# Performance work log

Measured on AMD Instinct MI355X. Metric: run time of the kernel, lower is better.

## Reference

```python
import jax, jax.numpy as jnp
import numpy as np

N = 100000
E = 1600000
IN_DIM = 128
HEADS = 4
OUT_DIM = 32


def setup_inputs() -> dict:
    key = jax.random.key(0)
    k1, k2, k3, k4, k5 = jax.random.split(key, 5)
    x = jax.random.normal(k1, (N, IN_DIM), dtype=jnp.float32)
    edge_index = jax.random.randint(k2, (2, E), 0, N, dtype=jnp.int64)
    # torch Linear weight: (out_features, in_features) = (HEADS*OUT_DIM, IN_DIM)
    W = jax.random.normal(k3, (HEADS * OUT_DIM, IN_DIM), dtype=jnp.float32) * 0.05
    a_src = jax.random.normal(k4, (HEADS, OUT_DIM), dtype=jnp.float32)
    a_dst = jax.random.normal(k5, (HEADS, OUT_DIM), dtype=jnp.float32)
    return {"x": x, "edge_index": edge_index, "W": W, "a_src": a_src, "a_dst": a_dst}


def reference(x, edge_index, W, a_src, a_dst):
    n = x.shape[0]
    H, D = a_src.shape
    # h: (N, H, D)
    h = (x @ W.T).reshape(n, H, D)
    src, dst = edge_index[0], edge_index[1]
    # per-edge attention logits: (E, H)
    e_src = jnp.einsum('ehd,hd->eh', h[src], a_src)
    e_dst = jnp.einsum('ehd,hd->eh', h[dst], a_dst)
    e = jax.nn.leaky_relu(e_src + e_dst, negative_slope=0.2)
    # segment max per destination node (init zeros, include_self=True as in torch)
    e_max = jnp.zeros((n, H), dtype=x.dtype).at[dst].max(e)
    e_exp = jnp.exp(e - e_max[dst])
    e_sum = jnp.zeros((n, H), dtype=x.dtype).at[dst].add(e_exp)
    alpha = e_exp / (e_sum[dst] + 1e-8)  # (E, H)
    # weighted messages and scatter-add aggregation
    msg = h[src] * alpha[..., None]  # (E, H, D)
    out = jnp.zeros((n, H, D), dtype=x.dtype).at[dst].add(msg)
    return out.reshape(n, H * D)  # concat=True
```

## Files before the change

### kernel.cpp

```cpp
#include <hip/hip_runtime.h>

#define IN_DIM 128
#define HD 128
#define HEADS 4
#define MD 64
#define CAP 128
#define NCOHORT 8
#define CHUNK 2048
#define NBMAX 512

typedef float nf4  __attribute__((ext_vector_type(4)));
typedef unsigned short nu4 __attribute__((ext_vector_type(4)));

__device__ __forceinline__ float lrelu(float v){ return v > 0.f ? v : 0.2f*v; }
__device__ __forceinline__ float4 add4(float4 a, float4 b){
  return make_float4(a.x+b.x, a.y+b.y, a.z+b.z, a.w+b.w);
}
__device__ __forceinline__ float4 expl4(float4 v){
  return make_float4(__expf(lrelu(v.x)), __expf(lrelu(v.y)), __expf(lrelu(v.z)), __expf(lrelu(v.w)));
}
__device__ __forceinline__ unsigned short f2b(float f){
  unsigned u = __float_as_uint(f);
  return (unsigned short)((u + 0x7FFFu + ((u >> 16) & 1u)) >> 16);
}
__device__ __forceinline__ float b2f(unsigned short b){
  return __uint_as_float(((unsigned)b) << 16);
}
__device__ __forceinline__ float blo(unsigned u){ return __uint_as_float(u << 16); }
__device__ __forceinline__ float bhi(unsigned u){ return __uint_as_float(u & 0xFFFF0000u); }

__global__ __launch_bounds__(256) void k_init(const float* __restrict__ W, float* __restrict__ WT){
  int idx = blockIdx.x*256 + threadIdx.x;
  int j = idx >> 7, k = idx & 127;
  WT[k*128 + j] = W[idx];
}

__global__ __launch_bounds__(256) void k_gemm_only(
    const float* __restrict__ x, const float* __restrict__ WT,
    const float* __restrict__ a_src, const float* __restrict__ a_dst,
    unsigned short* __restrict__ h, float* __restrict__ s, float* __restrict__ t,
    int n_nodes){
  __shared__ float xs[32][132];
  const int tid = threadIdx.x;
  const int base = blockIdx.x*32;
  if (base >= n_nodes) return;
  const int jg  = tid & 31;
  const int ng  = tid >> 5;
  const int j4  = jg*4;
  const float4 as4 = *(const float4*)(a_src + j4);
  const float4 ad4 = *(const float4*)(a_dst + j4);

  for (int i = tid; i < 32*32; i += 256){
    int row = i >> 5, c4 = (i & 31)*4;
    nf4 v = {0.f,0.f,0.f,0.f};
    if (base + row < n_nodes)
      v = __builtin_nontemporal_load((const nf4*)(x + (size_t)(base+row)*IN_DIM + c4));
    *(nf4*)&xs[row][c4] = v;
  }
  __syncthreads();

  float acc[4][4];
  #pragma unroll
  for (int i=0;i<4;++i){ acc[i][0]=acc[i][1]=acc[i][2]=acc[i][3]=0.f; }
  const int nb = ng*4;
  const float* wp = WT + j4;

  float4 wc0 = *(const float4*)(wp);
  float4 wc1 = *(const float4*)(wp + 128);
  float4 wc2 = *(const float4*)(wp + 256);
  float4 wc3 = *(const float4*)(wp + 384);
  for (int k=0;k<128;k+=4){
    const float* wq = wp + (size_t)(((k+4) & 127))*128;
    float4 wn0 = *(const float4*)(wq);
    float4 wn1 = *(const float4*)(wq + 128);
    float4 wn2 = *(const float4*)(wq + 256);
    float4 wn3 = *(const float4*)(wq + 384);
    #pragma unroll
    for (int u=0;u<4;++u){
      float4 xv = *(const float4*)&xs[nb+u][k];
      acc[u][0] = fmaf(wc0.x, xv.x, acc[u][0]);
      acc[u][1] = fmaf(wc0.y, xv.x, acc[u][1]);
      acc[u][2] = fmaf(wc0.z, xv.x, acc[u][2]);
      acc[u][3] = fmaf(wc0.w, xv.x, acc[u][3]);
      acc[u][0] = fmaf(wc1.x, xv.y, acc[u][0]);
      acc[u][1] = fmaf(wc1.y, xv.y, acc[u][1]);
      acc[u][2] = fmaf(wc1.z, xv.y, acc[u][2]);
      acc[u][3] = fmaf(wc1.w, xv.y, acc[u][3]);
      acc[u][0] = fmaf(wc2.x, xv.z, acc[u][0]);
      acc[u][1] = fmaf(wc2.y, xv.z, acc[u][1]);
      acc[u][2] = fmaf(wc2.z, xv.z, acc[u][2]);
      acc[u][3] = fmaf(wc2.w, xv.z, acc[u][3]);
      acc[u][0] = fmaf(wc3.x, xv.w, acc[u][0]);
      acc[u][1] = fmaf(wc3.y, xv.w, acc[u][1]);
      acc[u][2] = fmaf(wc3.z, xv.w, acc[u][2]);
      acc[u][3] = fmaf(wc3.w, xv.w, acc[u][3]);
    }
    wc0 = wn0; wc1 = wn1; wc2 = wn2; wc3 = wn3;
  }

  #pragma unroll
  for (int i=0;i<4;++i){
    int node = base + nb + i;
    if (node < n_nodes){
      nu4 hv = { f2b(acc[i][0]), f2b(acc[i][1]), f2b(acc[i][2]), f2b(acc[i][3]) };
      __builtin_nontemporal_store(hv, (nu4*)(h + (size_t)node*HD + j4));
    }
  }
  #pragma unroll
  for (int i=0;i<4;++i){
    float ps = acc[i][0]*as4.x + acc[i][1]*as4.y + acc[i][2]*as4.z + acc[i][3]*as4.w;
    float pt = acc[i][0]*ad4.x + acc[i][1]*ad4.y + acc[i][2]*ad4.z + acc[i][3]*ad4.w;
    ps += __shfl_xor(ps,1,64); ps += __shfl_xor(ps,2,64); ps += __shfl_xor(ps,4,64);
    pt += __shfl_xor(pt,1,64); pt += __shfl_xor(pt,2,64); pt += __shfl_xor(pt,4,64);
    if ((jg & 7) == 0){
      int node = base + nb + i;
      if (node < n_nodes){
        int hh = jg >> 3;
        s[node*HEADS + hh] = ps;
        t[node*HEADS + hh] = pt;
      }
    }
  }
}

__global__ __launch_bounds__(256) void k_bcount(const int* __restrict__ edst, int E_,
                                                int* __restrict__ cmat, int NB){
  __shared__ int hist[NBMAX];
  const int tid = threadIdx.x;
  for (int b = tid; b < NB; b += 256) hist[b] = 0;
  __syncthreads();
  const int base = blockIdx.x*CHUNK;
  const int lim  = (base + CHUNK < E_) ? base + CHUNK : E_;
  for (int i = base + tid; i < lim; i += 256)
    atomicAdd(&hist[((unsigned)edst[i]) >> 8], 1);
  __syncthreads();
  for (int b = tid; b < NB; b += 256)
    cmat[(size_t)blockIdx.x*NB + b] = hist[b];
}

__global__ __launch_bounds__(256) void k_bscan(int* __restrict__ cmat, int NCH, int NB,
                                               int* __restrict__ btot){
  const int lane = threadIdx.x & 63;
  const int b = blockIdx.x*4 + (threadIdx.x >> 6);
  if (b >= NB) return;
  int run = 0;
  for (int c0 = 0; c0 < NCH; c0 += 64){
    int c = c0 + lane;
    int v = (c < NCH) ? cmat[(size_t)c*NB + b] : 0;
    int incl = v;
    #pragma unroll
    for (int o=1;o<64;o<<=1){ int u = __shfl_up(incl, o, 64); if (lane >= o) incl += u; }
    if (c < NCH) cmat[(size_t)c*NB + b] = run + incl - v;
    run += __shfl(incl, 63, 64);
  }
  if (lane == 0) btot[b] = run;
}

__global__ __launch_bounds__(64) void k_bbase(const int* __restrict__ btot, int NB,
                                              int* __restrict__ bbase){
  const int lane = threadIdx.x;
  int run = 0;
  for (int c0 = 0; c0 < NB; c0 += 64){
    int c = c0 + lane;
    int v = (c < NB) ? btot[c] : 0;
    int incl = v;
    #pragma unroll
    for (int o=1;o<64;o<<=1){ int u = __shfl_up(incl, o, 64); if (lane >= o) incl += u; }
    if (c < NB) bbase[c] = run + incl - v;
    run += __shfl(incl, 63, 64);
  }
  if (lane == 0) bbase[NB] = run;
}

__global__ __launch_bounds__(256) void k_bscatter(const int* __restrict__ esrc,
    const int* __restrict__ edst, int E_, const int* __restrict__ cmat,
    const int* __restrict__ bbase, int* __restrict__ bucketbuf, int NB){
  __shared__ int cur[NBMAX];
  const int tid = threadIdx.x;
  for (int b = tid; b < NB; b += 256)
    cur[b] = bbase[b] + cmat[(size_t)blockIdx.x*NB + b];
  __syncthreads();
  const int base = blockIdx.x*CHUNK;
  const int lim  = (base + CHUNK < E_) ? base + CHUNK : E_;
  for (int i = base + tid; i < lim; i += 256){
    unsigned d = (unsigned)edst[i];
    int b = d >> 8;
    int pos = atomicAdd(&cur[b], 1);
    bucketbuf[pos] = esrc[i] | ((int)(d & 255u) << 24);
  }
}

__global__ __launch_bounds__(256) void k_bslots(const int* __restrict__ bucketbuf,
    const int* __restrict__ bbase, int* __restrict__ slots, int* __restrict__ count,
    int n_nodes){
  __shared__ int ncnt[256];
  const int tid = threadIdx.x;
  const int b = blockIdx.x;
  const int lo = bbase[b], hi = bbase[b+1];
  ncnt[tid] = 0;
  __syncthreads();
  for (int i = lo + tid; i < hi; i += 256)
    atomicAdd(&ncnt[((unsigned)bucketbuf[i]) >> 24], 1);
  __syncthreads();
  int node = b*256 + tid;
  if (node < n_nodes) count[node] = ncnt[tid];
  __syncthreads();
  ncnt[tid] = 0;
  __syncthreads();
  for (int i = lo + tid; i < hi; i += 256){
    int p = bucketbuf[i];
    int ld = ((unsigned)p) >> 24;
    int pos = atomicAdd(&ncnt[ld], 1);
    if (pos < MD) slots[(size_t)(b*256 + ld)*MD + pos] = p & 0xFFFFFF;
  }
}

__global__ __launch_bounds__(256) void k_aggregate2(const int* __restrict__ slots,
    const int* __restrict__ count, const unsigned short* __restrict__ h,
    const float* __restrict__ s, const float* __restrict__ t,
    float* __restrict__ out, int n_nodes){
  __shared__ int   s_src[4][MD];
  __shared__ float s_exp[4][MD][4];
  const int lane = threadIdx.x & 63;
  const int slot = threadIdx.x >> 6;
  const int n = blockIdx.x*4 + slot;
  if (n >= n_nodes) return;
  int cnt = count[n]; if (cnt > MD) cnt = MD;
  const float4 t4 = *(const float4*)(t + n*HEADS);

  float4 z4 = make_float4(0.f,0.f,0.f,0.f);
  if (lane < cnt){
    int src = slots[(size_t)n*MD + lane];
    s_src[slot][lane] = src;
    float4 s4 = *(const float4*)(s + src*HEADS);
    float4 e4 = expl4(add4(s4, t4));
    z4 = e4;
    *(float4*)&s_exp[slot][lane][0] = e4;
  }
  #pragma unroll
  for (int o=1;o<64;o<<=1){
    z4.x += __shfl_xor(z4.x,o,64);
    z4.y += __shfl_xor(z4.y,o,64);
    z4.z += __shfl_xor(z4.z,o,64);
    z4.w += __shfl_xor(z4.w,o,64);
  }

  const int qtr = lane >> 4;
  const int q   = lane & 15;
  const int hd  = q >> 2;
  float zh = hd==0 ? z4.x : hd==1 ? z4.y : hd==2 ? z4.z : z4.w;
  const float r = 1.f/(zh + 1e-8f);
  float4 accA = make_float4(0.f,0.f,0.f,0.f);
  float4 accB = make_float4(0.f,0.f,0.f,0.f);
  const unsigned short* hq = h + 8*q;

#define FMA8(U, W) \
  accA.x = fmaf(W, blo(U.x), accA.x); accA.y = fmaf(W, bhi(U.x), accA.y); \
  accA.z = fmaf(W, blo(U.y), accA.z); accA.w = fmaf(W, bhi(U.y), accA.w); \
  accB.x = fmaf(W, blo(U.z), accB.x); accB.y = fmaf(W, bhi(U.z), accB.y); \
  accB.z = fmaf(W, blo(U.w), accB.z); accB.w = fmaf(W, bhi(U.w), accB.w);

  int i = 0;
  for (; i + 8 <= cnt; i += 8){
    int eA = i + qtr, eB = i + 4 + qtr;
    int aA = s_src[slot][eA], aB = s_src[slot][eB];
    uint4 uA = *(const uint4*)(hq + (size_t)aA*HD);
    uint4 uB = *(const uint4*)(hq + (size_t)aB*HD);
    float wA = s_exp[slot][eA][hd], wB = s_exp[slot][eB][hd];
    FMA8(uA, wA); FMA8(uB, wB);
  }
  if (i + 4 <= cnt){
    int eA = i + qtr;
    int aA = s_src[slot][eA];
    uint4 uA = *(const uint4*)(hq + (size_t)aA*HD);
    float wA = s_exp[slot][eA][hd];
    FMA8(uA, wA);
    i += 4;
  }
  if (i < cnt && qtr < cnt - i){
    int eA = i + qtr;
    int aA = s_src[slot][eA];
    uint4 uA = *(const uint4*)(hq + (size_t)aA*HD);
    float wA = s_exp[slot][eA][hd];
    FMA8(uA, wA);
  }
#undef FMA8

  #pragma unroll
  for (int o=16;o<64;o<<=1){
    accA.x += __shfl_xor(accA.x,o,64); accA.y += __shfl_xor(accA.y,o,64);
    accA.z += __shfl_xor(accA.z,o,64); accA.w += __shfl_xor(accA.w,o,64);
    accB.x += __shfl_xor(accB.x,o,64); accB.y += __shfl_xor(accB.y,o,64);
    accB.z += __shfl_xor(accB.z,o,64); accB.w += __shfl_xor(accB.w,o,64);
  }
  if (qtr == 0){
    *(float4*)(out + (size_t)n*HD + 8*q)     = make_float4(accA.x*r, accA.y*r, accA.z*r, accA.w*r);
    *(float4*)(out + (size_t)n*HD + 8*q + 4) = make_float4(accB.x*r, accB.y*r, accB.z*r, accB.w*r);
  }
}

__global__ __launch_bounds__(256) void k_gemm(const float* __restrict__ x, const float* __restrict__ WT,
    const float* __restrict__ a_src, const float* __restrict__ a_dst,
    unsigned short* __restrict__ h, float* __restrict__ s, float* __restrict__ t,
    int n_nodes, int n_tiles){
  __shared__ float xs[64][132];
  const int tid = threadIdx.x;
  const int jg  = tid & 31;
  const int ng  = tid >> 5;
  const int j4  = jg*4;
  const float4 as4 = *(const float4*)(a_src + j4);
  const float4 ad4 = *(const float4*)(a_dst + j4);

  for (int tile = blockIdx.x; tile < n_tiles; tile += gridDim.x){
    const int base = tile*64;
    __syncthreads();
    for (int i = tid; i < 64*32; i += 256){
      int row = i >> 5, c4 = (i & 31)*4;
      float4 v = make_float4(0.f,0.f,0.f,0.f);
      if (base + row < n_nodes) v = *(const float4*)(x + (size_t)(base+row)*IN_DIM + c4);
      *(float4*)&xs[row][c4] = v;
    }
    __syncthreads();

    float acc[8][4];
    #pragma unroll
    for (int i=0;i<8;++i){ acc[i][0]=acc[i][1]=acc[i][2]=acc[i][3]=0.f; }
    const int nb = ng*8;
    for (int k=0;k<128;k+=4){
      float4 w0 = *(const float4*)(WT + (k  )*128 + j4);
      float4 w1 = *(const float4*)(WT + (k+1)*128 + j4);
      float4 w2 = *(const float4*)(WT + (k+2)*128 + j4);
      float4 w3 = *(const float4*)(WT + (k+3)*128 + j4);
      #pragma unroll
      for (int i=0;i<8;++i){
        float4 xv = *(const float4*)&xs[nb+i][k];
        acc[i][0] = fmaf(w0.x, xv.x, acc[i][0]); acc[i][1] = fmaf(w0.y, xv.x, acc[i][1]);
        acc[i][2] = fmaf(w0.z, xv.x, acc[i][2]); acc[i][3] = fmaf(w0.w, xv.x, acc[i][3]);
        acc[i][0] = fmaf(w1.x, xv.y, acc[i][0]); acc[i][1] = fmaf(w1.y, xv.y, acc[i][1]);
        acc[i][2] = fmaf(w1.z, xv.y, acc[i][2]); acc[i][3] = fmaf(w1.w, xv.y, acc[i][3]);
        acc[i][0] = fmaf(w2.x, xv.z, acc[i][0]); acc[i][1] = fmaf(w2.y, xv.z, acc[i][1]);
        acc[i][2] = fmaf(w2.z, xv.z, acc[i][2]); acc[i][3] = fmaf(w2.w, xv.z, acc[i][3]);
        acc[i][0] = fmaf(w3.x, xv.w, acc[i][0]); acc[i][1] = fmaf(w3.y, xv.w, acc[i][1]);
        acc[i][2] = fmaf(w3.z, xv.w, acc[i][2]); acc[i][3] = fmaf(w3.w, xv.w, acc[i][3]);
      }
    }
    #pragma unroll
    for (int i=0;i<8;++i){
      int node = base + nb + i;
      if (node < n_nodes)
        *(ushort4*)(h + (size_t)node*HD + j4) =
          make_ushort4(f2b(acc[i][0]), f2b(acc[i][1]), f2b(acc[i][2]), f2b(acc[i][3]));
    }
    #pragma unroll
    for (int i=0;i<8;++i){
      float ps = acc[i][0]*as4.x + acc[i][1]*as4.y + acc[i][2]*as4.z + acc[i][3]*as4.w;
      float pt = acc[i][0]*ad4.x + acc[i][1]*ad4.y + acc[i][2]*ad4.z + acc[i][3]*ad4.w;
      ps += __shfl_xor(ps,1,64); ps += __shfl_xor(ps,2,64); ps += __shfl_xor(ps,4,64);
      pt += __shfl_xor(pt,1,64); pt += __shfl_xor(pt,2,64); pt += __shfl_xor(pt,4,64);
      if ((jg & 7) == 0){
        int node = base + nb + i;
        if (node < n_nodes){
          int hh = jg >> 3;
          s[node*HEADS + hh] = ps;
          t[node*HEADS + hh] = pt;
        }
      }
    }
  }
}

__global__ __launch_bounds__(256) void k_hist(const int* __restrict__ dst, int E_,
                                              int* __restrict__ count, int R){
  const int c  = blockIdx.x & (NCOHORT-1);
  const int g  = (blockIdx.x >> 3)*256 + threadIdx.x;
  const int gs = (gridDim.x >> 3)*256;
  const unsigned lo = (unsigned)(c*R);
  for (int e = g; e < E_; e += gs){
    unsigned d = (unsigned)dst[e];
    if (d - lo < (unsigned)R) atomicAdd(&count[d], 1);
  }
}

__global__ void k_offsets(const int* __restrict__ count, int n_nodes,
                          int* __restrict__ offs, int* __restrict__ wcur, int* __restrict__ cursor){
  int n = blockIdx.x*blockDim.x + threadIdx.x;
  int lane = threadIdx.x & 63;
  int c = (n < n_nodes) ? count[n] : 0;
  int incl = c;
  #pragma unroll
  for (int o=1;o<64;o<<=1){
    int v = __shfl_up(incl, o, 64);
    if (lane >= o) incl += v;
  }
  int wave_total = __shfl(incl, 63, 64);
  int base = 0;
  if (lane == 63) base = atomicAdd(cursor, wave_total);
  base = __shfl(base, 63, 64);
  if (n < n_nodes){
    int off = base + incl - c;
    offs[n] = off; wcur[n] = off;
  }
}

__global__ __launch_bounds__(256) void k_scatter(const int* __restrict__ src, const int* __restrict__ dst,
                                                 int E_, int* __restrict__ wcur,
                                                 int* __restrict__ csr_src, int R){
  const int c  = blockIdx.x & (NCOHORT-1);
  const int g  = (blockIdx.x >> 3)*256 + threadIdx.x;
  const int gs = (gridDim.x >> 3)*256;
  const unsigned lo = (unsigned)(c*R);
  for (int e = g; e < E_; e += gs){
    unsigned d = (unsigned)dst[e];
    if (d - lo < (unsigned)R){
      int pos = atomicAdd(&wcur[d], 1);
      csr_src[pos] = src[e];
    }
  }
}

__global__ __launch_bounds__(256) void k_aggregate(const int* __restrict__ csr_src,
    const int* __restrict__ offs, const int* __restrict__ count,
    const unsigned short* __restrict__ h, const float* __restrict__ s, const float* __restrict__ t,
    float* __restrict__ out, int n_nodes){
  __shared__ int   s_src[4][CAP];
  __shared__ float s_exp[4][CAP][4];
  const int lane = threadIdx.x & 63;
  const int slot = threadIdx.x >> 6;
  const int n = blockIdx.x*4 + slot;
  if (n >= n_nodes) return;
  const int start = offs[n];
  const int cnt   = count[n];
  const float4 t4 = *(const float4*)(t + n*HEADS);
  const bool fast = (cnt <= CAP);

  float4 z4 = make_float4(0.f,0.f,0.f,0.f);
  if (fast){
    #pragma unroll
    for (int j=0;j<2;++j){
      int i = lane + j*64;
      if (i < cnt){
        int src = csr_src[start+i];
        s_src[slot][i] = src;
        float4 s4 = *(const float4*)(s + src*HEADS);
        float4 e4 = expl4(add4(s4, t4));
        z4 = add4(z4, e4);
        *(float4*)&s_exp[slot][i][0] = e4;
      }
    }
  } else {
    for (int i = lane; i < cnt; i += 64){
      int src = csr_src[start+i];
      float4 s4 = *(const float4*)(s + src*HEADS);
      z4 = add4(z4, expl4(add4(s4, t4)));
    }
  }
  #pragma unroll
  for (int o=1;o<64;o<<=1){
    z4.x += __shfl_xor(z4.x,o,64);
    z4.y += __shfl_xor(z4.y,o,64);
    z4.z += __shfl_xor(z4.z,o,64);
    z4.w += __shfl_xor(z4.w,o,64);
  }

  if (fast){
    const int half = lane >> 5;
    const int fl   = lane & 31;
    const int hd   = fl >> 3;
    float zh = hd==0 ? z4.x : hd==1 ? z4.y : hd==2 ? z4.z : z4.w;
    const float r = 1.f/(zh + 1e-8f);
    float4 acc = make_float4(0.f,0.f,0.f,0.f);
    int i = 0;
    for (; i + 4 <= cnt; i += 4){
      int a0 = s_src[slot][i+half], a1 = s_src[slot][i+2+half];
      ushort4 u0 = *(const ushort4*)(h + (size_t)a0*HD + 4*fl);
      ushort4 u1 = *(const ushort4*)(h + (size_t)a1*HD + 4*fl);
      float e0 = s_exp[slot][i+half][hd], e1 = s_exp[slot][i+2+half][hd];
      acc.x = fmaf(e0, b2f(u0.x), acc.x); acc.y = fmaf(e0, b2f(u0.y), acc.y);
      acc.z = fmaf(e0, b2f(u0.z), acc.z); acc.w = fmaf(e0, b2f(u0.w), acc.w);
      acc.x = fmaf(e1, b2f(u1.x), acc.x); acc.y = fmaf(e1, b2f(u1.y), acc.y);
      acc.z = fmaf(e1, b2f(u1.z), acc.z); acc.w = fmaf(e1, b2f(u1.w), acc.w);
    }
    if (i + 2 <= cnt){
      int a0 = s_src[slot][i+half];
      ushort4 u0 = *(const ushort4*)(h + (size_t)a0*HD + 4*fl);
      float e0 = s_exp[slot][i+half][hd];
      acc.x = fmaf(e0, b2f(u0.x), acc.x); acc.y = fmaf(e0, b2f(u0.y), acc.y);
      acc.z = fmaf(e0, b2f(u0.z), acc.z); acc.w = fmaf(e0, b2f(u0.w), acc.w);
      i += 2;
    }
    if (i < cnt && half == 0){
      int a0 = s_src[slot][i];
      ushort4 u0 = *(const ushort4*)(h + (size_t)a0*HD + 4*fl);
      float e0 = s_exp[slot][i][hd];
      acc.x = fmaf(e0, b2f(u0.x), acc.x); acc.y = fmaf(e0, b2f(u0.y), acc.y);
      acc.z = fmaf(e0, b2f(u0.z), acc.z); acc.w = fmaf(e0, b2f(u0.w), acc.w);
    }
    acc.x += __shfl_xor(acc.x, 32, 64);
    acc.y += __shfl_xor(acc.y, 32, 64);
    acc.z += __shfl_xor(acc.z, 32, 64);
    acc.w += __shfl_xor(acc.w, 32, 64);
    if (half == 0){
      *(float4*)(out + (size_t)n*HD + 4*fl) = make_float4(acc.x*r, acc.y*r, acc.z*r, acc.w*r);
    }
  } else {
    const int hd = lane >> 4;
    float zh = hd==0 ? z4.x : hd==1 ? z4.y : hd==2 ? z4.z : z4.w;
    const float r = 1.f/(zh + 1e-8f);
    float th = hd==0 ? t4.x : hd==1 ? t4.y : hd==2 ? t4.z : t4.w;
    float2 acc = make_float2(0.f,0.f);
    for (int i = 0; i < cnt; ++i){
      int src = csr_src[start+i];
      float4 s4 = *(const float4*)(s + src*HEADS);
      float sh = hd==0 ? s4.x : hd==1 ? s4.y : hd==2 ? s4.z : s4.w;
      float e = __expf(lrelu(sh+th));
      ushort2 u = *(const ushort2*)(h + (size_t)src*HD + 2*lane);
      acc.x = fmaf(e, b2f(u.x), acc.x); acc.y = fmaf(e, b2f(u.y), acc.y);
    }
    *(float2*)(out + (size_t)n*HD + 2*lane) = make_float2(acc.x*r, acc.y*r);
  }
}

extern "C" void kernel_launch(void* const* d_in, const int* in_sizes, int n_in,
                              void* d_out, int out_size, void* d_ws, size_t ws_size,
                              hipStream_t stream) {
  const float* x     = (const float*)d_in[0];
  const int*   ei    = (const int*)d_in[1];
  const float* W     = (const float*)d_in[2];
  const float* a_src = (const float*)d_in[3];
  const float* a_dst = (const float*)d_in[4];
  float* out = (float*)d_out;

  const int n_nodes = in_sizes[0] / IN_DIM;
  const int E_      = in_sizes[1] / 2;
  const int R       = (n_nodes + NCOHORT - 1) / NCOHORT;
  const int NB      = (n_nodes + 255) >> 8;
  const int NCH     = (E_ + CHUNK - 1) / CHUNK;

  char* ws = (char*)d_ws;
  size_t off = 0;
  auto alloc = [&](size_t bytes){ size_t cur = off; off += (bytes + 255) & ~255ULL; return cur; };

  float*          WT = (float*)(ws + alloc(128*128*4));
  unsigned short* h  = (unsigned short*)(ws + alloc((size_t)n_nodes*HD*2));
  float*          s  = (float*)(ws + alloc((size_t)n_nodes*HEADS*4));
  float*          t  = (float*)(ws + alloc((size_t)n_nodes*HEADS*4));

  size_t ms_need = off
    + (((size_t)n_nodes*4       + 255) & ~255ULL)
    + (((size_t)n_nodes*MD*4    + 255) & ~255ULL)
    + (((size_t)NCH*NB*4        + 255) & ~255ULL)
    + (((size_t)NB*4            + 255) & ~255ULL)
    + (((size_t)(NB+1)*4        + 255) & ~255ULL)
    + (((size_t)E_*4            + 255) & ~255ULL);

  if (ws_size >= ms_need && NB <= NBMAX && n_nodes < (1 << 24)){
    int* count     = (int*)(ws + alloc((size_t)n_nodes*4));
    int* slots     = (int*)(ws + alloc((size_t)n_nodes*MD*4));
    int* cmat      = (int*)(ws + alloc((size_t)NCH*NB*4));
    int* btot      = (int*)(ws + alloc((size_t)NB*4));
    int* bbase     = (int*)(ws + alloc((size_t)(NB+1)*4));
    int* bucketbuf = (int*)(ws + alloc((size_t)E_*4));

    k_init<<<64, 256, 0, stream>>>(W, WT);
    k_gemm_only<<<(n_nodes+31)/32, 256, 0, stream>>>(x, WT, a_src, a_dst, h, s, t, n_nodes);
    k_bcount<<<NCH, 256, 0, stream>>>(ei + E_, E_, cmat, NB);
    k_bscan<<<(NB+3)/4, 256, 0, stream>>>(cmat, NCH, NB, btot);
    k_bbase<<<1, 64, 0, stream>>>(btot, NB, bbase);
    k_bscatter<<<NCH, 256, 0, stream>>>(ei, ei + E_, E_, cmat, bbase, bucketbuf, NB);
    k_bslots<<<NB, 256, 0, stream>>>(bucketbuf, bbase, slots, count, n_nodes);
    k_aggregate2<<<(n_nodes+3)/4, 256, 0, stream>>>(slots, count, h, s, t, out, n_nodes);
  } else {
    int* count   = (int*)(ws + alloc((size_t)n_nodes*4));
    int* offs    = (int*)(ws + alloc((size_t)n_nodes*4));
    int* wcur    = (int*)(ws + alloc((size_t)n_nodes*4));
    int* cursor  = (int*)(ws + alloc(4));
    int* csr_src = (int*)(ws + alloc((size_t)E_*4));
    const int n_tiles = (n_nodes + 63) / 64;

    hipMemsetAsync(count, 0, (size_t)n_nodes*4, stream);
    hipMemsetAsync(cursor, 0, 4, stream);
    k_init<<<64, 256, 0, stream>>>(W, WT);
    k_gemm<<<n_tiles, 256, 0, stream>>>(x, WT, a_src, a_dst, h, s, t, n_nodes, n_tiles);
    k_hist<<<2048, 256, 0, stream>>>(ei + E_, E_, count, R);
    k_offsets<<<(n_nodes+255)/256, 256, 0, stream>>>(count, n_nodes, offs, wcur, cursor);
    k_scatter<<<2048, 256, 0, stream>>>(ei, ei + E_, E_, wcur, csr_src, R);
    k_aggregate<<<(n_nodes+3)/4, 256, 0, stream>>>(csr_src, offs, count, h, s, t, out, n_nodes);
  }
}
```

Before: 200.6 us.

## Interleave GEMM tiles into bucket-sort kernels and fold bbase scan into consumers

The standalone GEMM kernel is split into tiles and distributed across the four bucket-sort phase kernels as extra blocks. The GEMM work then runs alongside the latency-bound histogram, scan, scatter and slot kernels, filling idle compute units. The separate single-block bbase scan kernel is removed, and each scatter and slots block recomputes the bucket base prefix in shared memory. This saves launches but adds redundant per-block scans and extra shared memory that may lower occupancy.

```diff
diff --git a/kernel.cpp b/kernel.cpp
--- a/kernel.cpp
+++ b/kernel.cpp
@@ -35,14 +35,12 @@
   WT[k*128 + j] = W[idx];
 }
 
-__global__ __launch_bounds__(256) void k_gemm_only(
+__device__ __forceinline__ void gemm_tile(int tile,
     const float* __restrict__ x, const float* __restrict__ WT,
     const float* __restrict__ a_src, const float* __restrict__ a_dst,
     unsigned short* __restrict__ h, float* __restrict__ s, float* __restrict__ t,
-    int n_nodes){
-  __shared__ float xs[32][132];
-  const int tid = threadIdx.x;
-  const int base = blockIdx.x*32;
+    int n_nodes, float (*xs)[132], int tid){
+  const int base = tile*32;
   if (base >= n_nodes) return;
   const int jg  = tid & 31;
   const int ng  = tid >> 5;
@@ -123,95 +121,137 @@
   }
 }
 
-__global__ __launch_bounds__(256) void k_bcount(const int* __restrict__ edst, int E_,
-                                                int* __restrict__ cmat, int NB){
+__device__ __forceinline__ void scan_bbase(const int* __restrict__ btot, int NB,
+                                           int* bb, int tid){
+  if (tid < 64){
+    int run = 0;
+    for (int c0 = 0; c0 < NB; c0 += 64){
+      int c = c0 + tid;
+      int v = (c < NB) ? btot[c] : 0;
+      int incl = v;
+      #pragma unroll
+      for (int o=1;o<64;o<<=1){ int u = __shfl_up(incl, o, 64); if (tid >= o) incl += u; }
+      if (c < NB) bb[c] = run + incl - v;
+      run += __shfl(incl, 63, 64);
+    }
+    if (tid == 0) bb[NB] = run;
+  }
+  __syncthreads();
+}
+
+__global__ __launch_bounds__(256) void k_p1(const int* __restrict__ edst, int E_,
+    int* __restrict__ cmat, int NB, int NCH,
+    const float* __restrict__ x, const float* __restrict__ WT,
+    const float* __restrict__ a_src, const float* __restrict__ a_dst,
+    unsigned short* __restrict__ h, float* __restrict__ s, float* __restrict__ t,
+    int n_nodes, int g_base){
+  __shared__ float xs[32][132];
   __shared__ int hist[NBMAX];
   const int tid = threadIdx.x;
-  for (int b = tid; b < NB; b += 256) hist[b] = 0;
-  __syncthreads();
-  const int base = blockIdx.x*CHUNK;
-  const int lim  = (base + CHUNK < E_) ? base + CHUNK : E_;
-  for (int i = base + tid; i < lim; i += 256)
-    atomicAdd(&hist[((unsigned)edst[i]) >> 8], 1);
-  __syncthreads();
-  for (int b = tid; b < NB; b += 256)
-    cmat[(size_t)blockIdx.x*NB + b] = hist[b];
-}
-
-__global__ __launch_bounds__(256) void k_bscan(int* __restrict__ cmat, int NCH, int NB,
-                                               int* __restrict__ btot){
-  const int lane = threadIdx.x & 63;
-  const int b = blockIdx.x*4 + (threadIdx.x >> 6);
-  if (b >= NB) return;
-  int run = 0;
-  for (int c0 = 0; c0 < NCH; c0 += 64){
-    int c = c0 + lane;
-    int v = (c < NCH) ? cmat[(size_t)c*NB + b] : 0;
-    int incl = v;
-    #pragma unroll
-    for (int o=1;o<64;o<<=1){ int u = __shfl_up(incl, o, 64); if (lane >= o) incl += u; }
-    if (c < NCH) cmat[(size_t)c*NB + b] = run + incl - v;
-    run += __shfl(incl, 63, 64);
-  }
-  if (lane == 0) btot[b] = run;
-}
-
-__global__ __launch_bounds__(64) void k_bbase(const int* __restrict__ btot, int NB,
-                                              int* __restrict__ bbase){
-  const int lane = threadIdx.x;
-  int run = 0;
-  for (int c0 = 0; c0 < NB; c0 += 64){
-    int c = c0 + lane;
-    int v = (c < NB) ? btot[c] : 0;
-    int incl = v;
-    #pragma unroll
-    for (int o=1;o<64;o<<=1){ int u = __shfl_up(incl, o, 64); if (lane >= o) incl += u; }
-    if (c < NB) bbase[c] = run + incl - v;
-    run += __shfl(incl, 63, 64);
-  }
-  if (lane == 0) bbase[NB] = run;
-}
-
-__global__ __launch_bounds__(256) void k_bscatter(const int* __restrict__ esrc,
+  if ((int)blockIdx.x < NCH){
+    for (int b = tid; b < NB; b += 256) hist[b] = 0;
+    __syncthreads();
+    const int base = blockIdx.x*CHUNK;
+    const int lim  = (base + CHUNK < E_) ? base + CHUNK : E_;
+    for (int i = base + tid; i < lim; i += 256)
+      atomicAdd(&hist[((unsigned)edst[i]) >> 8], 1);
+    __syncthreads();
+    for (int b = tid; b < NB; b += 256)
+      cmat[(size_t)blockIdx.x*NB + b] = hist[b];
+  } else {
+    gemm_tile(g_base + (int)blockIdx.x - NCH, x, WT, a_src, a_dst, h, s, t, n_nodes, xs, tid);
+  }
+}
+
+__global__ __launch_bounds__(256) void k_p2(int* __restrict__ cmat, int NCH, int NB,
+    int* __restrict__ btot, int NBS,
+    const float* __restrict__ x, const float* __restrict__ WT,
+    const float* __restrict__ a_src, const float* __restrict__ a_dst,
+    unsigned short* __restrict__ h, float* __restrict__ s, float* __restrict__ t,
+    int n_nodes, int g_base){
+  __shared__ float xs[32][132];
+  const int tid = threadIdx.x;
+  if ((int)blockIdx.x < NBS){
+    const int lane = tid & 63;
+    const int b = blockIdx.x*4 + (tid >> 6);
+    if (b >= NB) return;
+    int run = 0;
+    for (int c0 = 0; c0 < NCH; c0 += 64){
+      int c = c0 + lane;
+      int v = (c < NCH) ? cmat[(size_t)c*NB + b] : 0;
+      int incl = v;
+      #pragma unroll
+      for (int o=1;o<64;o<<=1){ int u = __shfl_up(incl, o, 64); if (lane >= o) incl += u; }
+      if (c < NCH) cmat[(size_t)c*NB + b] = run + incl - v;
+      run += __shfl(incl, 63, 64);
+    }
+    if (lane == 0) btot[b] = run;
+  } else {
+    gemm_tile(g_base + (int)blockIdx.x - NBS, x, WT, a_src, a_dst, h, s, t, n_nodes, xs, tid);
+  }
+}
+
+__global__ __launch_bounds__(256) void k_p3(const int* __restrict__ esrc,
     const int* __restrict__ edst, int E_, const int* __restrict__ cmat,
-    const int* __restrict__ bbase, int* __restrict__ bucketbuf, int NB){
-  __shared__ int cur[NBMAX];
+    const int* __restrict__ btot, int* __restrict__ bucketbuf, int NB, int NCH,
+    const float* __restrict__ x, const float* __restrict__ WT,
+    const float* __restrict__ a_src, const float* __restrict__ a_dst,
+    unsigned short* __restrict__ h, float* __restrict__ s, float* __restrict__ t,
+    int n_nodes, int g_base){
+  __shared__ float xs[32][132];
+  __shared__ int bb[NBMAX+1];
   const int tid = threadIdx.x;
-  for (int b = tid; b < NB; b += 256)
-    cur[b] = bbase[b] + cmat[(size_t)blockIdx.x*NB + b];
-  __syncthreads();
-  const int base = blockIdx.x*CHUNK;
-  const int lim  = (base + CHUNK < E_) ? base + CHUNK : E_;
-  for (int i = base + tid; i < lim; i += 256){
-    unsigned d = (unsigned)edst[i];
-    int b = d >> 8;
-    int pos = atomicAdd(&cur[b], 1);
-    bucketbuf[pos] = esrc[i] | ((int)(d & 255u) << 24);
-  }
-}
-
-__global__ __launch_bounds__(256) void k_bslots(const int* __restrict__ bucketbuf,
-    const int* __restrict__ bbase, int* __restrict__ slots, int* __restrict__ count,
-    int n_nodes){
+  if ((int)blockIdx.x < NCH){
+    scan_bbase(btot, NB, bb, tid);
+    for (int b = tid; b < NB; b += 256)
+      bb[b] += cmat[(size_t)blockIdx.x*NB + b];
+    __syncthreads();
+    const int base = blockIdx.x*CHUNK;
+    const int lim  = (base + CHUNK < E_) ? base + CHUNK : E_;
+    for (int i = base + tid; i < lim; i += 256){
+      unsigned d = (unsigned)edst[i];
+      int b = d >> 8;
+      int pos = atomicAdd(&bb[b], 1);
+      bucketbuf[pos] = esrc[i] | ((int)(d & 255u) << 24);
+    }
+  } else {
+    gemm_tile(g_base + (int)blockIdx.x - NCH, x, WT, a_src, a_dst, h, s, t, n_nodes, xs, tid);
+  }
+}
+
+__global__ __launch_bounds__(256) void k_p4(const int* __restrict__ bucketbuf,
+    const int* __restrict__ btot, int* __restrict__ slots, int* __restrict__ count,
+    int n_nodes, int NB,
+    const float* __restrict__ x, const float* __restrict__ WT,
+    const float* __restrict__ a_src, const float* __restrict__ a_dst,
+    unsigned short* __restrict__ h, float* __restrict__ s, float* __restrict__ t,
+    int g_base){
+  __shared__ float xs[32][132];
+  __shared__ int bb[NBMAX+1];
   __shared__ int ncnt[256];
   const int tid = threadIdx.x;
-  const int b = blockIdx.x;
-  const int lo = bbase[b], hi = bbase[b+1];
-  ncnt[tid] = 0;
-  __syncthreads();
-  for (int i = lo + tid; i < hi; i += 256)
-    atomicAdd(&ncnt[((unsigned)bucketbuf[i]) >> 24], 1);
-  __syncthreads();
-  int node = b*256 + tid;
-  if (node < n_nodes) count[node] = ncnt[tid];
-  __syncthreads();
-  ncnt[tid] = 0;
-  __syncthreads();
-  for (int i = lo + tid; i < hi; i += 256){
-    int p = bucketbuf[i];
-    int ld = ((unsigned)p) >> 24;
-    int pos = atomicAdd(&ncnt[ld], 1);
-    if (pos < MD) slots[(size_t)(b*256 + ld)*MD + pos] = p & 0xFFFFFF;
+  if ((int)blockIdx.x < NB){
+    scan_bbase(btot, NB, bb, tid);
+    const int b = blockIdx.x;
+    const int lo = bb[b], hi = bb[b] + btot[b];
+    ncnt[tid] = 0;
+    __syncthreads();
+    for (int i = lo + tid; i < hi; i += 256)
+      atomicAdd(&ncnt[((unsigned)bucketbuf[i]) >> 24], 1);
+    __syncthreads();
+    int node = b*256 + tid;
+    if (node < n_nodes) count[node] = ncnt[tid];
+    __syncthreads();
+    ncnt[tid] = 0;
+    __syncthreads();
+    for (int i = lo + tid; i < hi; i += 256){
+      int p = bucketbuf[i];
+      int ld = ((unsigned)p) >> 24;
+      int pos = atomicAdd(&ncnt[ld], 1);
+      if (pos < MD) slots[(size_t)(b*256 + ld)*MD + pos] = p & 0xFFFFFF;
+    }
+  } else {
+    gemm_tile(g_base + (int)blockIdx.x - NB, x, WT, a_src, a_dst, h, s, t, n_nodes, xs, tid);
   }
 }
 
@@ -535,6 +575,7 @@
   const int R       = (n_nodes + NCOHORT - 1) / NCOHORT;
   const int NB      = (n_nodes + 255) >> 8;
   const int NCH     = (E_ + CHUNK - 1) / CHUNK;
+  const int NBS     = (NB + 3) / 4;
 
   char* ws = (char*)d_ws;
   size_t off = 0;
@@ -550,7 +591,6 @@
     + (((size_t)n_nodes*MD*4    + 255) & ~255ULL)
     + (((size_t)NCH*NB*4        + 255) & ~255ULL)
     + (((size_t)NB*4            + 255) & ~255ULL)
-    + (((size_t)(NB+1)*4        + 255) & ~255ULL)
     + (((size_t)E_*4            + 255) & ~255ULL);
 
   if (ws_size >= ms_need && NB <= NBMAX && n_nodes < (1 << 24)){
@@ -558,16 +598,21 @@
     int* slots     = (int*)(ws + alloc((size_t)n_nodes*MD*4));
     int* cmat      = (int*)(ws + alloc((size_t)NCH*NB*4));
     int* btot      = (int*)(ws + alloc((size_t)NB*4));
-    int* bbase     = (int*)(ws + alloc((size_t)(NB+1)*4));
     int* bucketbuf = (int*)(ws + alloc((size_t)E_*4));
 
+    const int NG = (n_nodes + 31) / 32;
+    int G1 = (NG*38)/100, G2 = (NG*10)/100, G3 = (NG*35)/100;
+    int G4 = NG - G1 - G2 - G3;
+
     k_init<<<64, 256, 0, stream>>>(W, WT);
-    k_gemm_only<<<(n_nodes+31)/32, 256, 0, stream>>>(x, WT, a_src, a_dst, h, s, t, n_nodes);
-    k_bcount<<<NCH, 256, 0, stream>>>(ei + E_, E_, cmat, NB);
-    k_bscan<<<(NB+3)/4, 256, 0, stream>>>(cmat, NCH, NB, btot);
-    k_bbase<<<1, 64, 0, stream>>>(btot, NB, bbase);
-    k_bscatter<<<NCH, 256, 0, stream>>>(ei, ei + E_, E_, cmat, bbase, bucketbuf, NB);
-    k_bslots<<<NB, 256, 0, stream>>>(bucketbuf, bbase, slots, count, n_nodes);
+    k_p1<<<NCH + G1, 256, 0, stream>>>(ei + E_, E_, cmat, NB, NCH,
+        x, WT, a_src, a_dst, h, s, t, n_nodes, 0);
+    k_p2<<<NBS + G2, 256, 0, stream>>>(cmat, NCH, NB, btot, NBS,
+        x, WT, a_src, a_dst, h, s, t, n_nodes, G1);
+    k_p3<<<NCH + G3, 256, 0, stream>>>(ei, ei + E_, E_, cmat, btot, bucketbuf, NB, NCH,
+        x, WT, a_src, a_dst, h, s, t, n_nodes, G1 + G2);
+    k_p4<<<NB + G4, 256, 0, stream>>>(bucketbuf, btot, slots, count, n_nodes, NB,
+        x, WT, a_src, a_dst, h, s, t, G1 + G2 + G3);
     k_aggregate2<<<(n_nodes+3)/4, 256, 0, stream>>>(slots, count, h, s, t, out, n_nodes);
   } else {
     int* count   = (int*)(ws + alloc((size_t)n_nodes*4));
```

Measured after the change: 187.2 us (median of 2 runs). -6.7%, faster.
